# Optimization experiments

Measured on AMD Instinct MI355X. Metric: run time of the kernel, lower is better.

The kernel has to match this reference:

```python
import jax, jax.numpy as jnp
import numpy as np
import math

B, S, HID = 2, 2048, 2048
H, HK, D = 16, 4, 128          # query heads, kv heads, head_dim
R = 64                         # rope_dim = head_dim * partial_rotary_factor
EPS = 1e-6
THETA = 10000.0


def _rope_tables():
    inv_freq = 1.0 / (THETA ** (np.arange(0, R, 2, dtype=np.float32) / R))
    t = np.arange(S, dtype=np.float32)
    freqs = np.outer(t, inv_freq)                      # [S, R/2]
    emb = np.concatenate([freqs, freqs], axis=-1)      # [S, R]
    cos = np.broadcast_to(np.cos(emb)[None], (B, S, R)).copy()
    sin = np.broadcast_to(np.sin(emb)[None], (B, S, R)).copy()
    return jnp.asarray(cos), jnp.asarray(sin)


def setup_inputs() -> dict:
    key = jax.random.key(0)
    ks = jax.random.split(key, 3)
    cos, sin = _rope_tables()
    return {
        "hidden_states": jax.random.normal(ks[0], (B, S, HID), dtype=jnp.float32),
        "cos": cos,
        "sin": sin,
        "w_qkv": jax.random.normal(ks[1], ((H + 2 * HK) * D, HID), dtype=jnp.float32) * (HID ** -0.5),
        "q_ln_w": jnp.ones((D,), dtype=jnp.float32),
        "k_ln_w": jnp.ones((D,), dtype=jnp.float32),
        "w_dense": jax.random.normal(ks[2], (HID, H * D), dtype=jnp.float32) * ((H * D) ** -0.5),
    }


def _rms_norm(x, w):
    xf = x.astype(jnp.float32)
    var = jnp.mean(xf * xf, axis=-1, keepdims=True)
    return w * (xf * jax.lax.rsqrt(var + EPS)).astype(x.dtype)


def _rotate_half(x):
    x1, x2 = x[..., : x.shape[-1] // 2], x[..., x.shape[-1] // 2 :]
    return jnp.concatenate([-x2, x1], axis=-1)


def _apply_rope(q, k, cos, sin):
    # cos/sin: [B, S, R] -> [B, 1, S, R]; partial rotary on first R dims
    cos = cos[:, None, :, :]
    sin = sin[:, None, :, :]
    q_rot, q_pass = q[..., :R], q[..., R:]
    k_rot, k_pass = k[..., :R], k[..., R:]
    q_emb = q_rot * cos + _rotate_half(q_rot) * sin
    k_emb = k_rot * cos + _rotate_half(k_rot) * sin
    return (jnp.concatenate([q_emb, q_pass], axis=-1),
            jnp.concatenate([k_emb, k_pass], axis=-1))


def reference(hidden_states, cos, sin, w_qkv, q_ln_w, k_ln_w, w_dense):
    bsz, q_len, _ = hidden_states.shape
    qkv = jnp.einsum('bsh,oh->bso', hidden_states, w_qkv)            # [B,S,(H+2HK)*D]
    qkv = qkv.reshape(bsz, q_len, H + 2 * HK, D)
    q, k, v = jnp.split(qkv, [H, H + HK], axis=2)
    q = jnp.transpose(q, (0, 2, 1, 3))                               # [B,H,S,D]
    k = jnp.transpose(k, (0, 2, 1, 3))                               # [B,HK,S,D]
    v = jnp.transpose(v, (0, 2, 1, 3))

    q = _rms_norm(q, q_ln_w)
    k = _rms_norm(k, k_ln_w)
    q, k = _apply_rope(q, k, cos, sin)

    n_rep = H // HK
    k = jnp.repeat(k, n_rep, axis=1)                                 # [B,H,S,D]
    v = jnp.repeat(v, n_rep, axis=1)

    scores = jnp.einsum('bhqd,bhkd->bhqk', q, k) / math.sqrt(D)
    probs = jax.nn.softmax(scores.astype(jnp.float32), axis=-1).astype(q.dtype)
    attn = jnp.einsum('bhqk,bhkd->bhqd', probs, v)                   # [B,H,S,D]
    attn = jnp.transpose(attn, (0, 2, 1, 3)).reshape(bsz, q_len, H * D)
    return jnp.einsum('bsd,od->bso', attn, w_dense)                  # [B,S,HID]
```

## Files before the change

kernel.cpp:

```cpp
#include <hip/hip_runtime.h>
#include <hip/hip_bf16.h>
#include <math.h>

#define B_   2
#define S_   2048
#define HID_ 2048
#define H_   16
#define HK_  4
#define D_   128
#define NH_  24
#define QKVN 3072
#define R_   64

typedef __attribute__((ext_vector_type(8))) _Float16 h8;
typedef __attribute__((ext_vector_type(4))) _Float16 h4;
typedef __attribute__((ext_vector_type(2))) _Float16 h2;
typedef __attribute__((ext_vector_type(4))) float f4;

#define GLOAD16(gp, lp) __builtin_amdgcn_global_load_lds(                      \
    (const __attribute__((address_space(1))) void*)(gp),                       \
    (__attribute__((address_space(3))) void*)(lp), 16, 0, 0)

__global__ __launch_bounds__(256) void cvt3(
    const float* __restrict__ s0, _Float16* __restrict__ d0, int n0,
    const float* __restrict__ s1, _Float16* __restrict__ d1, int n1,
    const float* __restrict__ s2, _Float16* __restrict__ d2, int n2)
{
    int j = blockIdx.x * 256 + threadIdx.x;
    const float* s; _Float16* d;
    if (j < n0) { s = s0; d = d0; }
    else {
        j -= n0;
        if (j < n1) { s = s1; d = d1; }
        else { j -= n1; if (j >= n2) return; s = s2; d = d2; }
    }
    float4 a = ((const float4*)s)[j * 2];
    float4 b = ((const float4*)s)[j * 2 + 1];
    h8 h;
    h[0] = (_Float16)a.x; h[1] = (_Float16)a.y;
    h[2] = (_Float16)a.z; h[3] = (_Float16)a.w;
    h[4] = (_Float16)b.x; h[5] = (_Float16)b.y;
    h[6] = (_Float16)b.z; h[7] = (_Float16)b.w;
    ((h8*)d)[j] = h;
}

__global__ __launch_bounds__(256, 4) void gemm_qkv(
    const _Float16* __restrict__ A, const _Float16* __restrict__ Bm,
    const float* __restrict__ cosT, const float* __restrict__ sinT,
    const float* __restrict__ qw, const float* __restrict__ kw,
    _Float16* __restrict__ Qh_g, _Float16* __restrict__ Kh_g,
    _Float16* __restrict__ Vt_g)
{
    __shared__ char smem_raw[34816];
    auto Ast  = (_Float16 (*)[128][32])(smem_raw);
    auto Bst  = (_Float16 (*)[128][32])(smem_raw + 16384);
    auto exch = (float (*)[128])(smem_raw + 32768);

    const int tid = threadIdx.x;
    const int wave = tid >> 6, lane = tid & 63;
    const int l15 = lane & 15, l4 = lane >> 4;
    const int h  = blockIdx.x;
    const int m0 = blockIdx.y * 128;
    const int n0 = h * 128;
    const int wm = (wave >> 1) * 64, wn = (wave & 1) * 64;
    const int K = HID_;

    f4 acc[16];
#pragma unroll
    for (int t = 0; t < 16; ++t) acc[t] = (f4){0.f, 0.f, 0.f, 0.f};

    const int srow = lane >> 2;
    const int gsrc = (((lane & 3) ^ (srow & 3)) * 8);
    const int rkey = l15 & 3;

    auto STAGE = [&](int bf, int k0) {
#pragma unroll
        for (int t = 0; t < 2; ++t) {
            const int rbase = wave * 16 + 64 * t;
            const int grow  = rbase + srow;
            GLOAD16(A  + (size_t)(m0 + grow) * K + k0 + gsrc, &Ast[bf][rbase][0]);
            GLOAD16(Bm + (size_t)(n0 + grow) * K + k0 + gsrc, &Bst[bf][rbase][0]);
        }
    };

    STAGE(0, 0);
    int cur = 0;

    for (int k0 = 0; k0 < K; k0 += 32) {
        __syncthreads();
        if (k0 + 32 < K) STAGE(cur ^ 1, k0 + 32);

        h8 ahf[4], bhf[4];
#pragma unroll
        for (int i = 0; i < 4; ++i) {
            ahf[i] = *(const h8*)&Ast[cur][wm + i * 16 + l15][(l4 ^ rkey) * 8];
            bhf[i] = *(const h8*)&Bst[cur][wn + i * 16 + l15][(l4 ^ rkey) * 8];
        }
        __builtin_amdgcn_s_setprio(1);
#pragma unroll
        for (int i = 0; i < 4; ++i)
#pragma unroll
            for (int jj = 0; jj < 4; ++jj)
                acc[i * 4 + jj] = __builtin_amdgcn_mfma_f32_16x16x32_f16(
                    ahf[i], bhf[jj], acc[i * 4 + jj], 0, 0, 0);
        __builtin_amdgcn_s_setprio(0);
        cur ^= 1;
    }

    const int bb = m0 >> 11;
    const int s0 = m0 & 2047;

    if (h < 20) {
        float sq[4][4];
#pragma unroll
        for (int i = 0; i < 4; ++i)
#pragma unroll
            for (int r = 0; r < 4; ++r) {
                float s = 0.f;
#pragma unroll
                for (int jj = 0; jj < 4; ++jj) {
                    float v = acc[i * 4 + jj][r];
                    s += v * v;
                }
                s += __shfl_xor(s, 1);
                s += __shfl_xor(s, 2);
                s += __shfl_xor(s, 4);
                s += __shfl_xor(s, 8);
                sq[i][r] = s;
            }
        const int half = wave & 1;
        if (l15 == 0) {
#pragma unroll
            for (int i = 0; i < 4; ++i)
#pragma unroll
                for (int r = 0; r < 4; ++r)
                    exch[half][wm + i * 16 + l4 * 4 + r] = sq[i][r];
        }
        __syncthreads();

        const float* wln = (h < 16) ? qw : kw;
        float wv[4];
#pragma unroll
        for (int jj = 0; jj < 4; ++jj) wv[jj] = wln[wn + jj * 16 + l15];

        const float QS = 0.08838834764831845f * 1.4426950408889634f;
        _Float16 (*Ld)[128] = (_Float16 (*)[128])smem_raw;

#pragma unroll
        for (int i = 0; i < 4; ++i) {
#pragma unroll
            for (int r = 0; r < 4; ++r) {
                const int row = wm + i * 16 + l4 * 4 + r;
                const int s  = s0 + row;
                float tot = sq[i][r] + exch[half ^ 1][row];
                float scale = rsqrtf(tot * (1.f / 128.f) + 1e-6f);
                float y[4];
#pragma unroll
                for (int jj = 0; jj < 4; ++jj)
                    y[jj] = acc[i * 4 + jj][r] * scale * wv[jj];

                float yr[4];
                if (wn == 0) {
                    const float* cp = cosT + ((size_t)bb * S_ + s) * R_;
                    const float* sp = sinT + ((size_t)bb * S_ + s) * R_;
                    float cs[4], sn[4];
#pragma unroll
                    for (int jj = 0; jj < 4; ++jj) {
                        cs[jj] = cp[jj * 16 + l15];
                        sn[jj] = sp[jj * 16 + l15];
                    }
                    yr[0] = y[0] * cs[0] - y[2] * sn[0];
                    yr[1] = y[1] * cs[1] - y[3] * sn[1];
                    yr[2] = y[2] * cs[2] + y[0] * sn[2];
                    yr[3] = y[3] * cs[3] + y[1] * sn[3];
                } else {
#pragma unroll
                    for (int jj = 0; jj < 4; ++jj) yr[jj] = y[jj];
                }

                const float os = (h < 16) ? QS : 1.f;
#pragma unroll
                for (int jj = 0; jj < 4; ++jj)
                    Ld[row][wn + jj * 16 + l15] = (_Float16)(yr[jj] * os);
            }
        }
        __syncthreads();

        _Float16* outb = (h < 16)
            ? Qh_g + (((size_t)bb * H_ + h) * S_ + s0) * D_
            : Kh_g + (((size_t)bb * HK_ + (h - 16)) * S_ + s0) * D_;
        const int rr = tid >> 4;
        const int d0 = (tid & 15) * 8;
#pragma unroll
        for (int it = 0; it < 8; ++it) {
            const int row = it * 16 + rr;
            *(h8*)(outb + (size_t)row * D_ + d0) = *(const h8*)&Ld[row][d0];
        }
    } else {
        const size_t vbase = ((size_t)bb * HK_ + (h - 20)) * D_ * S_;
#pragma unroll
        for (int i = 0; i < 4; ++i)
#pragma unroll
            for (int jj = 0; jj < 4; ++jj) {
                h4 pk;
#pragma unroll
                for (int r = 0; r < 4; ++r) pk[r] = (_Float16)acc[i * 4 + jj][r];
                const int d = wn + jj * 16 + l15;
                const int s = s0 + wm + i * 16 + l4 * 4;
                *(h4*)(Vt_g + vbase + (size_t)d * S_ + s) = pk;
            }
    }
}

__global__ __launch_bounds__(256, 4) void gemm_dense(
    const _Float16* __restrict__ A, const _Float16* __restrict__ Bm,
    float* __restrict__ Cv, int M, int N, int K)
{
    __shared__ _Float16 Ast[2][128][32];
    __shared__ _Float16 Bst[2][128][32];

    const int tid = threadIdx.x;
    const int wave = tid >> 6, lane = tid & 63;
    const int l15 = lane & 15, l4 = lane >> 4;
    const int m0 = blockIdx.y * 128, n0 = blockIdx.x * 128;
    const int wm = (wave >> 1) * 64, wn = (wave & 1) * 64;

    f4 acc[16];
#pragma unroll
    for (int t = 0; t < 16; ++t) acc[t] = (f4){0.f, 0.f, 0.f, 0.f};

    const int srow = lane >> 2;
    const int gsrc = (((lane & 3) ^ (srow & 3)) * 8);
    const int rkey = l15 & 3;

    auto STAGE = [&](int bf, int k0) {
#pragma unroll
        for (int t = 0; t < 2; ++t) {
            const int rbase = wave * 16 + 64 * t;
            const int grow  = rbase + srow;
            GLOAD16(A  + (size_t)(m0 + grow) * K + k0 + gsrc, &Ast[bf][rbase][0]);
            GLOAD16(Bm + (size_t)(n0 + grow) * K + k0 + gsrc, &Bst[bf][rbase][0]);
        }
    };

    STAGE(0, 0);
    int cur = 0;

    for (int k0 = 0; k0 < K; k0 += 32) {
        __syncthreads();
        if (k0 + 32 < K) STAGE(cur ^ 1, k0 + 32);

        h8 ahf[4], bhf[4];
#pragma unroll
        for (int i = 0; i < 4; ++i) {
            ahf[i] = *(const h8*)&Ast[cur][wm + i * 16 + l15][(l4 ^ rkey) * 8];
            bhf[i] = *(const h8*)&Bst[cur][wn + i * 16 + l15][(l4 ^ rkey) * 8];
        }
        __builtin_amdgcn_s_setprio(1);
#pragma unroll
        for (int i = 0; i < 4; ++i)
#pragma unroll
            for (int jj = 0; jj < 4; ++jj)
                acc[i * 4 + jj] = __builtin_amdgcn_mfma_f32_16x16x32_f16(
                    ahf[i], bhf[jj], acc[i * 4 + jj], 0, 0, 0);
        __builtin_amdgcn_s_setprio(0);
        cur ^= 1;
    }

#pragma unroll
    for (int i = 0; i < 4; ++i)
#pragma unroll
        for (int jj = 0; jj < 4; ++jj)
#pragma unroll
            for (int r = 0; r < 4; ++r) {
                int row = m0 + wm + i * 16 + l4 * 4 + r;
                int col = n0 + wn + jj * 16 + l15;
                Cv[(size_t)row * N + col] = acc[i * 4 + jj][r];
            }
}

__global__ __launch_bounds__(256, 2) void flash_mfma(
    const _Float16* __restrict__ Qh_g, const _Float16* __restrict__ Kh_g,
    const _Float16* __restrict__ Vt_g, _Float16* __restrict__ Ao)
{
    __shared__ _Float16 Ksh[2][64][128];
    __shared__ _Float16 Vsh[2][128][64];
    __shared__ _Float16 Ps [128][64];

    const int tid = threadIdx.x;
    const int wave = tid >> 6, lane = tid & 63;
    const int l15 = lane & 15, l4 = lane >> 4;
    const int qb = blockIdx.x, h = blockIdx.y, b = blockIdx.z;
    const int kh = h >> 2;
    const int key = l15 & 7;

    h8 qf[2][4];
#pragma unroll
    for (int i = 0; i < 2; ++i) {
        const _Float16* qrow = Qh_g +
            (((size_t)b * H_ + h) * S_ + qb * 128 + wave * 32 + i * 16 + l15) * D_;
#pragma unroll
        for (int j = 0; j < 4; ++j)
            qf[i][j] = *(const h8*)(qrow + j * 32 + l4 * 8);
    }

    f4 o[2][8];
#pragma unroll
    for (int i = 0; i < 2; ++i)
#pragma unroll
        for (int t = 0; t < 8; ++t) o[i][t] = (f4){0.f, 0.f, 0.f, 0.f};
    float l_part[2] = {0.f, 0.f};

    const size_t kvoff = ((size_t)b * HK_ + kh) * S_ * D_;
    const _Float16* kg = Kh_g + kvoff;
    const _Float16* vg = Vt_g + kvoff;

    int krow[4], ksrc[4], vrow[4], vsrc[4];
#pragma unroll
    for (int t = 0; t < 4; ++t) {
        krow[t] = wave * 16 + t * 4 + (lane >> 4);
        ksrc[t] = ((lane & 15) ^ (krow[t] & 7)) * 8;
        vrow[t] = wave * 32 + t * 8 + (lane >> 3);
        vsrc[t] = ((lane & 7) ^ (vrow[t] & 7)) * 8;
    }

    auto STAGE = [&](int bf, int kb) {
#pragma unroll
        for (int t = 0; t < 4; ++t)
            GLOAD16(kg + (size_t)(kb * 64 + krow[t]) * D_ + ksrc[t],
                    &Ksh[bf][wave * 16 + t * 4][0]);
#pragma unroll
        for (int t = 0; t < 4; ++t)
            GLOAD16(vg + (size_t)vrow[t] * S_ + kb * 64 + vsrc[t],
                    &Vsh[bf][wave * 32 + t * 8][0]);
    };

    STAGE(0, 0);
    int cur = 0;

    for (int kb = 0; kb < S_ / 64; ++kb) {
        __syncthreads();
        if (kb + 1 < S_ / 64) STAGE(cur ^ 1, kb + 1);

        f4 acc[4][2];
#pragma unroll
        for (int c = 0; c < 4; ++c)
#pragma unroll
            for (int i = 0; i < 2; ++i)
                acc[c][i] = (f4){-8.f, -8.f, -8.f, -8.f};
#pragma unroll
        for (int j = 0; j < 4; ++j) {
#pragma unroll
            for (int c = 0; c < 4; ++c) {
                h8 kf = *(const h8*)&Ksh[cur][c * 16 + l15][((j * 4 + l4) ^ key) * 8];
#pragma unroll
                for (int i = 0; i < 2; ++i)
                    acc[c][i] = __builtin_amdgcn_mfma_f32_16x16x32_f16(
                        kf, qf[i][j], acc[c][i], 0, 0, 0);
            }
        }

#pragma unroll
        for (int c = 0; c < 4; ++c) {
#pragma unroll
            for (int i = 0; i < 2; ++i) {
                h4 pk;
#pragma unroll
                for (int r = 0; r < 4; ++r) {
                    float e_ = exp2f(acc[c][i][r]);
                    l_part[i] += e_;
                    pk[r] = (_Float16)e_;
                }
                int g = 2 * c + (l4 >> 1);
                *(h4*)&Ps[wave * 32 + i * 16 + l15][(g ^ key) * 8 + (l4 & 1) * 4] = pk;
            }
        }

#pragma unroll
        for (int s2 = 0; s2 < 2; ++s2) {
            int gc = ((s2 * 4 + l4) ^ key) * 8;
            h8 pf0 = *(const h8*)&Ps[wave * 32 + l15][gc];
            h8 pf1 = *(const h8*)&Ps[wave * 32 + 16 + l15][gc];
#pragma unroll
            for (int t = 0; t < 8; ++t) {
                h8 vf = *(const h8*)&Vsh[cur][t * 16 + l15][gc];
                o[0][t] = __builtin_amdgcn_mfma_f32_16x16x32_f16(pf0, vf, o[0][t], 0, 0, 0);
                o[1][t] = __builtin_amdgcn_mfma_f32_16x16x32_f16(pf1, vf, o[1][t], 0, 0, 0);
            }
        }
        cur ^= 1;
    }

    float Linv[2];
#pragma unroll
    for (int i = 0; i < 2; ++i) {
        float l = l_part[i];
        l += __shfl_xor(l, 16);
        l += __shfl_xor(l, 32);
        Linv[i] = 1.f / l;
    }
#pragma unroll
    for (int i = 0; i < 2; ++i) {
        float inv[4];
#pragma unroll
        for (int r = 0; r < 4; ++r) inv[r] = __shfl(Linv[i], l4 * 4 + r);
#pragma unroll
        for (int t = 0; t < 8; ++t) {
#pragma unroll
            for (int r = 0; r < 4; ++r) {
                int row = qb * 128 + wave * 32 + i * 16 + l4 * 4 + r;
                Ao[((size_t)b * S_ + row) * (H_ * D_) + h * D_ + t * 16 + l15] =
                    (_Float16)(o[i][t][r] * inv[r]);
            }
        }
    }
}

extern "C" void kernel_launch(void* const* d_in, const int* in_sizes, int n_in,
                              void* d_out, int out_size, void* d_ws, size_t ws_size,
                              hipStream_t stream)
{
    const float* hidden  = (const float*)d_in[0];
    const float* cosT    = (const float*)d_in[1];
    const float* sinT    = (const float*)d_in[2];
    const float* w_qkv   = (const float*)d_in[3];
    const float* q_ln    = (const float*)d_in[4];
    const float* k_ln    = (const float*)d_in[5];
    const float* w_dense = (const float*)d_in[6];
    float* out = (float*)d_out;

    char* w = (char*)d_ws;
    _Float16* attn16   = (_Float16*)w;
    _Float16* hidden16 = (_Float16*)(w + 16777216);
    _Float16* wqkv16   = (_Float16*)(w + 33554432);
    _Float16* Qh       = (_Float16*)(w + 46137344);
    _Float16* Kh       = (_Float16*)(w + 62914560);
    _Float16* Vt       = (_Float16*)(w + 67108864);
    _Float16* wdense16 = (_Float16*)(w + 71303168);

    cvt3<<<9216, 256, 0, stream>>>(hidden,  hidden16, 1048576,
                                   w_qkv,   wqkv16,   786432,
                                   w_dense, wdense16, 524288);

    gemm_qkv<<<dim3(NH_, (B_ * S_) / 128), 256, 0, stream>>>(
        hidden16, wqkv16, cosT, sinT, q_ln, k_ln, Qh, Kh, Vt);

    flash_mfma<<<dim3(S_ / 128, H_, B_), 256, 0, stream>>>(Qh, Kh, Vt, attn16);

    gemm_dense<<<dim3(HID_ / 128, (B_ * S_) / 128), 256, 0, stream>>>(
        attn16, wdense16, out, B_ * S_, HID_, H_ * D_);
}
```

Before: 321.7 us.

## Switch flash attention to 32x32x16 MFMA with register-resident P via permlane swap

Rewrites the attention inner loop to use 32x32x16 MFMA tiles instead of 16x16x32. The softmax probabilities are packed to fp16 and rearranged in registers with v_permlane32_swap, so they no longer round-trip through the shared-memory Ps buffer. s_setprio is raised around the MFMA sections to favour matrix issue. This removes LDS traffic and frees LDS, at the cost of larger accumulator register use and more intricate lane-to-row mapping.

```diff
diff --git a/kernel.cpp b/kernel.cpp
--- a/kernel.cpp
+++ b/kernel.cpp
@@ -16,10 +16,17 @@
 typedef __attribute__((ext_vector_type(4))) _Float16 h4;
 typedef __attribute__((ext_vector_type(2))) _Float16 h2;
 typedef __attribute__((ext_vector_type(4))) float f4;
+typedef __attribute__((ext_vector_type(16))) float f16v;
+typedef __attribute__((ext_vector_type(4))) unsigned u4;
 
 #define GLOAD16(gp, lp) __builtin_amdgcn_global_load_lds(                      \
     (const __attribute__((address_space(1))) void*)(gp),                       \
     (__attribute__((address_space(3))) void*)(lp), 16, 0, 0)
+
+__device__ __forceinline__ unsigned pk16(float a, float b) {
+    auto v = __builtin_amdgcn_cvt_pkrtz(a, b);
+    return *reinterpret_cast<unsigned*>(&v);
+}
 
 __global__ __launch_bounds__(256) void cvt3(
     const float* __restrict__ s0, _Float16* __restrict__ d0, int n0,
@@ -285,31 +292,27 @@
 {
     __shared__ _Float16 Ksh[2][64][128];
     __shared__ _Float16 Vsh[2][128][64];
-    __shared__ _Float16 Ps [128][64];
 
     const int tid = threadIdx.x;
     const int wave = tid >> 6, lane = tid & 63;
-    const int l15 = lane & 15, l4 = lane >> 4;
-    const int qb = blockIdx.x, h = blockIdx.y, b = blockIdx.z;
-    const int kh = h >> 2;
-    const int key = l15 & 7;
-
-    h8 qf[2][4];
-#pragma unroll
-    for (int i = 0; i < 2; ++i) {
+    const int l31 = lane & 31, hw = lane >> 5;
+    const int qb = blockIdx.x, head = blockIdx.y, b = blockIdx.z;
+    const int kh = head >> 2;
+    const int key = lane & 7;
+
+    h8 qf[8];
+    {
         const _Float16* qrow = Qh_g +
-            (((size_t)b * H_ + h) * S_ + qb * 128 + wave * 32 + i * 16 + l15) * D_;
-#pragma unroll
-        for (int j = 0; j < 4; ++j)
-            qf[i][j] = *(const h8*)(qrow + j * 32 + l4 * 8);
-    }
-
-    f4 o[2][8];
-#pragma unroll
-    for (int i = 0; i < 2; ++i)
-#pragma unroll
-        for (int t = 0; t < 8; ++t) o[i][t] = (f4){0.f, 0.f, 0.f, 0.f};
-    float l_part[2] = {0.f, 0.f};
+            (((size_t)b * H_ + head) * S_ + qb * 128 + wave * 32 + l31) * D_;
+#pragma unroll
+        for (int j = 0; j < 8; ++j)
+            qf[j] = *(const h8*)(qrow + j * 16 + hw * 8);
+    }
+
+    f16v o[4];
+#pragma unroll
+    for (int t = 0; t < 4; ++t) o[t] = 0.f;
+    float lp = 0.f;
 
     const size_t kvoff = ((size_t)b * HK_ + kh) * S_ * D_;
     const _Float16* kg = Kh_g + kvoff;
@@ -342,76 +345,61 @@
         __syncthreads();
         if (kb + 1 < S_ / 64) STAGE(cur ^ 1, kb + 1);
 
-        f4 acc[4][2];
-#pragma unroll
-        for (int c = 0; c < 4; ++c)
-#pragma unroll
-            for (int i = 0; i < 2; ++i)
-                acc[c][i] = (f4){-8.f, -8.f, -8.f, -8.f};
-#pragma unroll
-        for (int j = 0; j < 4; ++j) {
-#pragma unroll
-            for (int c = 0; c < 4; ++c) {
-                h8 kf = *(const h8*)&Ksh[cur][c * 16 + l15][((j * 4 + l4) ^ key) * 8];
-#pragma unroll
-                for (int i = 0; i < 2; ++i)
-                    acc[c][i] = __builtin_amdgcn_mfma_f32_16x16x32_f16(
-                        kf, qf[i][j], acc[c][i], 0, 0, 0);
+        f16v a0 = -8.f, a1 = -8.f;
+        __builtin_amdgcn_s_setprio(1);
+#pragma unroll
+        for (int j = 0; j < 8; ++j) {
+            const int gc = ((2 * j + hw) ^ key) * 8;
+            h8 kf0 = *(const h8*)&Ksh[cur][l31][gc];
+            h8 kf1 = *(const h8*)&Ksh[cur][32 + l31][gc];
+            a0 = __builtin_amdgcn_mfma_f32_32x32x16_f16(kf0, qf[j], a0, 0, 0, 0);
+            a1 = __builtin_amdgcn_mfma_f32_32x32x16_f16(kf1, qf[j], a1, 0, 0, 0);
+        }
+        __builtin_amdgcn_s_setprio(0);
+
+#pragma unroll
+        for (int r = 0; r < 16; ++r) {
+            a0[r] = exp2f(a0[r]);  lp += a0[r];
+            a1[r] = exp2f(a1[r]);  lp += a1[r];
+        }
+
+        __builtin_amdgcn_s_setprio(1);
+#pragma unroll
+        for (int s = 0; s < 4; ++s) {
+            const f16v& pa = (s < 2) ? a0 : a1;
+            const int base = (s & 1) * 8;
+            unsigned d0 = pk16(pa[base + 0], pa[base + 1]);
+            unsigned d1 = pk16(pa[base + 2], pa[base + 3]);
+            unsigned d2 = pk16(pa[base + 4], pa[base + 5]);
+            unsigned d3 = pk16(pa[base + 6], pa[base + 7]);
+            asm volatile("v_permlane32_swap_b32 %0, %1" : "+v"(d0), "+v"(d2));
+            asm volatile("v_permlane32_swap_b32 %0, %1" : "+v"(d1), "+v"(d3));
+            u4 fw; fw.x = d0; fw.y = d1; fw.z = d2; fw.w = d3;
+            h8 pfrag = __builtin_bit_cast(h8, fw);
+
+            const int gv = ((2 * s + hw) ^ key) * 8;
+#pragma unroll
+            for (int t = 0; t < 4; ++t) {
+                h8 vf = *(const h8*)&Vsh[cur][t * 32 + l31][gv];
+                o[t] = __builtin_amdgcn_mfma_f32_32x32x16_f16(pfrag, vf, o[t], 0, 0, 0);
             }
         }
-
-#pragma unroll
-        for (int c = 0; c < 4; ++c) {
-#pragma unroll
-            for (int i = 0; i < 2; ++i) {
-                h4 pk;
-#pragma unroll
-                for (int r = 0; r < 4; ++r) {
-                    float e_ = exp2f(acc[c][i][r]);
-                    l_part[i] += e_;
-                    pk[r] = (_Float16)e_;
-                }
-                int g = 2 * c + (l4 >> 1);
-                *(h4*)&Ps[wave * 32 + i * 16 + l15][(g ^ key) * 8 + (l4 & 1) * 4] = pk;
-            }
-        }
-
-#pragma unroll
-        for (int s2 = 0; s2 < 2; ++s2) {
-            int gc = ((s2 * 4 + l4) ^ key) * 8;
-            h8 pf0 = *(const h8*)&Ps[wave * 32 + l15][gc];
-            h8 pf1 = *(const h8*)&Ps[wave * 32 + 16 + l15][gc];
-#pragma unroll
-            for (int t = 0; t < 8; ++t) {
-                h8 vf = *(const h8*)&Vsh[cur][t * 16 + l15][gc];
-                o[0][t] = __builtin_amdgcn_mfma_f32_16x16x32_f16(pf0, vf, o[0][t], 0, 0, 0);
-                o[1][t] = __builtin_amdgcn_mfma_f32_16x16x32_f16(pf1, vf, o[1][t], 0, 0, 0);
-            }
-        }
+        __builtin_amdgcn_s_setprio(0);
         cur ^= 1;
     }
 
-    float Linv[2];
-#pragma unroll
-    for (int i = 0; i < 2; ++i) {
-        float l = l_part[i];
-        l += __shfl_xor(l, 16);
-        l += __shfl_xor(l, 32);
-        Linv[i] = 1.f / l;
-    }
-#pragma unroll
-    for (int i = 0; i < 2; ++i) {
-        float inv[4];
-#pragma unroll
-        for (int r = 0; r < 4; ++r) inv[r] = __shfl(Linv[i], l4 * 4 + r);
-#pragma unroll
-        for (int t = 0; t < 8; ++t) {
-#pragma unroll
-            for (int r = 0; r < 4; ++r) {
-                int row = qb * 128 + wave * 32 + i * 16 + l4 * 4 + r;
-                Ao[((size_t)b * S_ + row) * (H_ * D_) + h * D_ + t * 16 + l15] =
-                    (_Float16)(o[i][t][r] * inv[r]);
-            }
+    float Linv = 1.f / (lp + __shfl_xor(lp, 32));
+
+    const size_t obase = (((size_t)b * S_ + qb * 128 + wave * 32) * (H_ * D_))
+                         + (size_t)head * D_;
+#pragma unroll
+    for (int r = 0; r < 16; ++r) {
+        const int qr = (r & 3) + 8 * (r >> 2) + 4 * hw;
+        float invr = __shfl(Linv, qr);
+#pragma unroll
+        for (int t = 0; t < 4; ++t) {
+            Ao[obase + (size_t)qr * (H_ * D_) + t * 32 + l31] =
+                (_Float16)(o[t][r] * invr);
         }
     }
 }
```

Result: slower. 329.5 us (+2.4%).
